# Performance work log

Measured on AMD Instinct MI355X. Metric: run time of the kernel, lower is better.

Reference implementation:

```python
import jax, jax.numpy as jnp
import numpy as np

B, N, D, H = 2, 512, 256, 256  # batch, seq_len, input_dim, hidden_dim
H2 = H // 2


def setup_inputs() -> dict:
    key = jax.random.key(0)
    ks = jax.random.split(key, 12)
    def lin(kw, kb, fan_in, fan_out):
        bound = 1.0 / np.sqrt(fan_in)
        W = jax.random.uniform(kw, (fan_in, fan_out), jnp.float32, -bound, bound)
        b = jax.random.uniform(kb, (fan_out,), jnp.float32, -bound, bound)
        return W, b
    W1, b1 = lin(ks[0], ks[1], 2 * D, H)
    W2, b2 = lin(ks[2], ks[3], H, H2)
    W3, b3 = lin(ks[4], ks[5], H2, 1)
    Wg, bg = lin(ks[6], ks[7], D, H)
    x = jax.random.normal(ks[8], (B, N, D), jnp.float32)
    base_adj = jax.random.uniform(ks[9], (B, N, N), jnp.float32)
    return {"x": x, "base_adj": base_adj, "W1": W1, "b1": b1,
            "W2": W2, "b2": b2, "W3": W3, "b3": b3, "Wg": Wg, "bg": bg}


def reference(x, base_adj, W1, b1, W2, b2, W3, b3, Wg, bg):
    # x: [B,N,D], base_adj: [B,N,N]
    Din = x.shape[-1]
    n = x.shape[1]
    # Linear on concat([x_i, x_j]) == x_i @ W1[:D] + x_j @ W1[D:]  (same math,
    # avoids materializing the [B,N,N,2D] pair tensor)
    left = jnp.einsum('bid,dh->bih', x, W1[:Din])    # [B,N,H]
    right = jnp.einsum('bjd,dh->bjh', x, W1[Din:])   # [B,N,H]
    h = jax.nn.relu(left[:, :, None, :] + right[:, None, :, :] + b1)  # [B,N,N,H]
    h = jax.nn.relu(jnp.einsum('bijh,hk->bijk', h, W2) + b2)          # [B,N,N,H/2]
    edge_weights = jax.nn.sigmoid(jnp.einsum('bijk,k->bij', h, W3[:, 0]) + b3[0])
    dynamic_adj = base_adj * edge_weights + jnp.eye(n, dtype=x.dtype)[None]
    dynamic_adj = jax.nn.softmax(dynamic_adj, axis=-1)
    agg = jnp.matmul(dynamic_adj, x)                 # [B,N,D]
    return jnp.einsum('bnd,dh->bnh', agg, Wg) + bg   # [B,N,H]
```

## Files before the change

### kernel.cpp

```cpp
#include <hip/hip_runtime.h>
#include <hip/hip_bf16.h>

#define NB 2
#define NN 512
#define ND 256
#define NH 256
#define NH2 128

#define JT 128
#define PADH 264

typedef __bf16 bf16x8 __attribute__((ext_vector_type(8)));
typedef float f32x4 __attribute__((ext_vector_type(4)));

__global__ __launch_bounds__(256) void prep_kernel(
    const float* __restrict__ x, const float* __restrict__ W1,
    const float* __restrict__ b1, const float* __restrict__ Wg,
    const float* __restrict__ bg, const float* __restrict__ W2,
    float* __restrict__ Lb, float* __restrict__ Rr, float* __restrict__ XW,
    __bf16* __restrict__ W2b) {
  const int blk = blockIdx.x;
  const int tid = threadIdx.x;
  if (blk >= 512) {
    const int idx = (blk - 512) * 256 + tid;
    const int k = idx >> 8;
    const int h = idx & 255;
    W2b[idx] = (__bf16)W2[h * NH2 + k];
    return;
  }
  __shared__ float xs[2][ND];
  const int r0 = blk * 2;
  xs[0][tid] = x[r0 * ND + tid];
  xs[1][tid] = x[(r0 + 1) * ND + tid];
  __syncthreads();

  float aL0 = 0.f, aL1 = 0.f, aR0 = 0.f, aR1 = 0.f, aG0 = 0.f, aG1 = 0.f;
  const int h = tid;
  for (int d = 0; d < ND; ++d) {
    const float wl = W1[d * NH + h];
    const float wr = W1[(ND + d) * NH + h];
    const float wg = Wg[d * NH + h];
    const float x0 = xs[0][d], x1 = xs[1][d];
    aL0 = fmaf(x0, wl, aL0); aL1 = fmaf(x1, wl, aL1);
    aR0 = fmaf(x0, wr, aR0); aR1 = fmaf(x1, wr, aR1);
    aG0 = fmaf(x0, wg, aG0); aG1 = fmaf(x1, wg, aG1);
  }
  const float bb1 = b1[h];
  const float bbg = bg[h];
  Lb[r0 * NH + h] = aL0 + bb1;       Lb[(r0 + 1) * NH + h] = aL1 + bb1;
  Rr[r0 * NH + h] = aR0;             Rr[(r0 + 1) * NH + h] = aR1;
  XW[r0 * NH + h] = aG0 + bbg;       XW[(r0 + 1) * NH + h] = aG1 + bbg;
}

__global__ __launch_bounds__(256, 2) void edge_kernel(
    const float* __restrict__ base_adj,
    const float* __restrict__ b2, const float* __restrict__ W3,
    const float* __restrict__ b3, const float* __restrict__ Lb,
    const float* __restrict__ Rr, const float* __restrict__ XW,
    const __bf16* __restrict__ W2b, float* __restrict__ out) {
  __shared__ __align__(16) __bf16 Hs[JT][PADH];
  __shared__ __align__(16) float Lbs[NH];
  __shared__ float b2s[NH2], W3s[NH2];
  __shared__ float ew[NN];
  __shared__ float red[2][JT];
  __shared__ float sred[8];

  const int bi = blockIdx.x;
  const int b = bi >> 9;
  const int i = bi & (NN - 1);
  const int tid = threadIdx.x;
  const int lane = tid & 63;
  const int w = tid >> 6;
  const int wy = w >> 1;
  const int wx = w & 1;
  const int lr = lane & 15;
  const int lg = lane >> 4;

  bf16x8 bfr[8][4];
  #pragma unroll
  for (int ks8 = 0; ks8 < 8; ++ks8)
    #pragma unroll
    for (int kb = 0; kb < 4; ++kb) {
      const int col = wx * 64 + kb * 16 + lr;
      bfr[ks8][kb] = *(const bf16x8*)(W2b + col * NH + ks8 * 32 + lg * 8);
    }

  Lbs[tid] = Lb[bi * NH + tid];
  if (tid < NH2) { b2s[tid] = b2[tid]; W3s[tid] = W3[tid]; }
  __syncthreads();

  const float* Rb = Rr + b * NN * NH;
  const float b3v = b3[0];

  for (int jt = 0; jt < NN; jt += JT) {
    #pragma unroll
    for (int it = 0; it < 16; ++it) {
      const int q = it * 256 + tid;
      const int jj = q >> 5;
      const int h8 = (q & 31) << 3;
      const f32x4 rv0 = *(const f32x4*)(Rb + (jt + jj) * NH + h8);
      const f32x4 rv1 = *(const f32x4*)(Rb + (jt + jj) * NH + h8 + 4);
      const f32x4 lv0 = *(const f32x4*)(Lbs + h8);
      const f32x4 lv1 = *(const f32x4*)(Lbs + h8 + 4);
      bf16x8 hv;
      #pragma unroll
      for (int e = 0; e < 4; ++e) {
        float t0 = rv0[e] + lv0[e];
        float t1 = rv1[e] + lv1[e];
        hv[e] = (__bf16)(t0 > 0.f ? t0 : 0.f);
        hv[e + 4] = (__bf16)(t1 > 0.f ? t1 : 0.f);
      }
      *(bf16x8*)(&Hs[jj][h8]) = hv;
    }
    __syncthreads();

    f32x4 acc[4][4];
    #pragma unroll
    for (int ja = 0; ja < 4; ++ja)
      #pragma unroll
      for (int kb = 0; kb < 4; ++kb) acc[ja][kb] = (f32x4){0.f, 0.f, 0.f, 0.f};

    const __bf16* Hp = &Hs[0][0];
    #pragma unroll
    for (int ks8 = 0; ks8 < 8; ++ks8) {
      bf16x8 af[4];
      #pragma unroll
      for (int ja = 0; ja < 4; ++ja) {
        const int row = wy * 64 + ja * 16 + lr;
        af[ja] = *(const bf16x8*)(Hp + row * PADH + ks8 * 32 + lg * 8);
      }
      #pragma unroll
      for (int ja = 0; ja < 4; ++ja)
        #pragma unroll
        for (int kb = 0; kb < 4; ++kb)
          acc[ja][kb] = __builtin_amdgcn_mfma_f32_16x16x32_bf16(af[ja], bfr[ks8][kb], acc[ja][kb], 0, 0, 0);
    }

    #pragma unroll
    for (int ja = 0; ja < 4; ++ja) {
      #pragma unroll
      for (int r = 0; r < 4; ++r) {
        float s = 0.f;
        #pragma unroll
        for (int kb = 0; kb < 4; ++kb) {
          const int k = wx * 64 + kb * 16 + lr;
          float t = acc[ja][kb][r] + b2s[k];
          t = t > 0.f ? t : 0.f;
          s = fmaf(t, W3s[k], s);
        }
        s += __shfl_xor(s, 1, 16);
        s += __shfl_xor(s, 2, 16);
        s += __shfl_xor(s, 4, 16);
        s += __shfl_xor(s, 8, 16);
        if (lr == 0) red[wx][wy * 64 + ja * 16 + lg * 4 + r] = s;
      }
    }
    __syncthreads();

    if (tid < JT) {
      const float v = red[0][tid] + red[1][tid] + b3v;
      const float sg = 1.f / (1.f + __expf(-v));
      const int j = jt + tid;
      ew[j] = base_adj[(b * NN + i) * NN + j] * sg + ((j == i) ? 1.f : 0.f);
    }
    __syncthreads();
  }

  float v0 = ew[tid], v1 = ew[tid + 256];
  float m = fmaxf(v0, v1);
  #pragma unroll
  for (int off = 1; off < 64; off <<= 1) m = fmaxf(m, __shfl_xor(m, off, 64));
  if (lane == 0) sred[w] = m;
  __syncthreads();
  m = fmaxf(fmaxf(sred[0], sred[1]), fmaxf(sred[2], sred[3]));
  const float e0 = __expf(v0 - m), e1 = __expf(v1 - m);
  float ssum = e0 + e1;
  #pragma unroll
  for (int off = 1; off < 64; off <<= 1) ssum += __shfl_xor(ssum, off, 64);
  if (lane == 0) sred[4 + w] = ssum;
  __syncthreads();
  const float inv = 1.f / (sred[4] + sred[5] + sred[6] + sred[7]);
  ew[tid] = e0 * inv;
  ew[tid + 256] = e1 * inv;
  __syncthreads();

  const float* XWb = XW + b * NN * NH;
  float o0 = 0.f, o1 = 0.f, o2 = 0.f, o3 = 0.f;
  for (int j = 0; j < NN; j += 4) {
    o0 = fmaf(ew[j + 0], XWb[(j + 0) * NH + tid], o0);
    o1 = fmaf(ew[j + 1], XWb[(j + 1) * NH + tid], o1);
    o2 = fmaf(ew[j + 2], XWb[(j + 2) * NH + tid], o2);
    o3 = fmaf(ew[j + 3], XWb[(j + 3) * NH + tid], o3);
  }
  out[bi * NH + tid] = (o0 + o1) + (o2 + o3);
}

extern "C" void kernel_launch(void* const* d_in, const int* in_sizes, int n_in,
                              void* d_out, int out_size, void* d_ws, size_t ws_size,
                              hipStream_t stream) {
  const float* x        = (const float*)d_in[0];
  const float* base_adj = (const float*)d_in[1];
  const float* W1       = (const float*)d_in[2];
  const float* b1       = (const float*)d_in[3];
  const float* W2       = (const float*)d_in[4];
  const float* b2       = (const float*)d_in[5];
  const float* W3       = (const float*)d_in[6];
  const float* b3       = (const float*)d_in[7];
  const float* Wg       = (const float*)d_in[8];
  const float* bg       = (const float*)d_in[9];

  float* Lb = (float*)d_ws;
  float* Rr = Lb + NB * NN * NH;
  float* XW = Rr + NB * NN * NH;
  __bf16* W2b = (__bf16*)(XW + NB * NN * NH);
  float* out = (float*)d_out;

  prep_kernel<<<512 + 128, 256, 0, stream>>>(x, W1, b1, Wg, bg, W2, Lb, Rr, XW, W2b);
  edge_kernel<<<NB * NN, 256, 0, stream>>>(base_adj, b2, W3, b3, Lb, Rr, XW, W2b, out);
}
```

Before: 202.5 us.

## Restructure edge kernel with bf16 intermediates, async LDS prefetch, smaller tiles

Stores the R projection and the XW aggregation operand as bf16, which halves their global traffic. The edge kernel now tiles j by 32 rows and double-buffers R tiles into LDS with global_load_lds prefetch, and it uses XOR-swizzled H rows to avoid bank conflicts. Each wave now owns a 32-column slice of the k dimension, which reduces register pressure so occupancy can rise to 4 blocks per CU. The prep kernel is vectorised over h with split-d partial sums, and base_adj is loaded up front. Rounding R and XW to bf16 adds some precision loss.

```diff
diff --git a/kernel.cpp b/kernel.cpp
--- a/kernel.cpp
+++ b/kernel.cpp
@@ -6,63 +6,105 @@
 #define ND 256
 #define NH 256
 #define NH2 128
-
-#define JT 128
-#define PADH 264
+#define JT 32
 
 typedef __bf16 bf16x8 __attribute__((ext_vector_type(8)));
+typedef __bf16 bf16x4 __attribute__((ext_vector_type(4)));
 typedef float f32x4 __attribute__((ext_vector_type(4)));
+
+__device__ __forceinline__ void gload_lds16(const void* g, void* l) {
+  __builtin_amdgcn_global_load_lds((const __attribute__((address_space(1))) unsigned int*)g,
+                                   (__attribute__((address_space(3))) unsigned int*)l, 16, 0, 0);
+}
+__device__ __forceinline__ float bflo(unsigned d) { return __uint_as_float(d << 16); }
+__device__ __forceinline__ float bfhi(unsigned d) { return __uint_as_float(d & 0xffff0000u); }
 
 __global__ __launch_bounds__(256) void prep_kernel(
     const float* __restrict__ x, const float* __restrict__ W1,
     const float* __restrict__ b1, const float* __restrict__ Wg,
     const float* __restrict__ bg, const float* __restrict__ W2,
-    float* __restrict__ Lb, float* __restrict__ Rr, float* __restrict__ XW,
-    __bf16* __restrict__ W2b) {
+    float* __restrict__ Lb, __bf16* __restrict__ Rb16,
+    __bf16* __restrict__ XWb16, __bf16* __restrict__ W2b) {
   const int blk = blockIdx.x;
   const int tid = threadIdx.x;
   if (blk >= 512) {
     const int idx = (blk - 512) * 256 + tid;
-    const int k = idx >> 8;
-    const int h = idx & 255;
-    W2b[idx] = (__bf16)W2[h * NH2 + k];
+    const int h = idx >> 7;
+    const int k = idx & 127;
+    W2b[k * NH + h] = (__bf16)W2[idx];
     return;
   }
   __shared__ float xs[2][ND];
+  __shared__ __align__(16) f32x4 part[4 * 384];
   const int r0 = blk * 2;
   xs[0][tid] = x[r0 * ND + tid];
   xs[1][tid] = x[(r0 + 1) * ND + tid];
   __syncthreads();
 
-  float aL0 = 0.f, aL1 = 0.f, aR0 = 0.f, aR1 = 0.f, aG0 = 0.f, aG1 = 0.f;
-  const int h = tid;
-  for (int d = 0; d < ND; ++d) {
-    const float wl = W1[d * NH + h];
-    const float wr = W1[(ND + d) * NH + h];
-    const float wg = Wg[d * NH + h];
+  const int dg = tid >> 6;
+  const int hq = tid & 63;
+  f32x4 acc[2][3];
+  #pragma unroll
+  for (int r = 0; r < 2; ++r)
+    #pragma unroll
+    for (int m = 0; m < 3; ++m) acc[r][m] = (f32x4){0.f, 0.f, 0.f, 0.f};
+
+  const int d0 = dg * 64;
+  for (int it = 0; it < 64; ++it) {
+    const int d = d0 + it;
+    const f32x4 wl = *(const f32x4*)(W1 + d * NH + hq * 4);
+    const f32x4 wr = *(const f32x4*)(W1 + (ND + d) * NH + hq * 4);
+    const f32x4 wg = *(const f32x4*)(Wg + d * NH + hq * 4);
     const float x0 = xs[0][d], x1 = xs[1][d];
-    aL0 = fmaf(x0, wl, aL0); aL1 = fmaf(x1, wl, aL1);
-    aR0 = fmaf(x0, wr, aR0); aR1 = fmaf(x1, wr, aR1);
-    aG0 = fmaf(x0, wg, aG0); aG1 = fmaf(x1, wg, aG1);
-  }
-  const float bb1 = b1[h];
-  const float bbg = bg[h];
-  Lb[r0 * NH + h] = aL0 + bb1;       Lb[(r0 + 1) * NH + h] = aL1 + bb1;
-  Rr[r0 * NH + h] = aR0;             Rr[(r0 + 1) * NH + h] = aR1;
-  XW[r0 * NH + h] = aG0 + bbg;       XW[(r0 + 1) * NH + h] = aG1 + bbg;
-}
-
-__global__ __launch_bounds__(256, 2) void edge_kernel(
+    acc[0][0] += x0 * wl;  acc[0][1] += x0 * wr;  acc[0][2] += x0 * wg;
+    acc[1][0] += x1 * wl;  acc[1][1] += x1 * wr;  acc[1][2] += x1 * wg;
+  }
+  #pragma unroll
+  for (int r = 0; r < 2; ++r)
+    #pragma unroll
+    for (int m = 0; m < 3; ++m)
+      part[dg * 384 + (r * 3 + m) * 64 + hq] = acc[r][m];
+  __syncthreads();
+
+  for (int s = tid; s < 384; s += 256) {
+    f32x4 sum = part[s] + part[384 + s] + part[768 + s] + part[1152 + s];
+    const int r = s / 192;
+    const int rem = s - r * 192;
+    const int m = rem >> 6;
+    const int h = (rem & 63) * 4;
+    const int row = r0 + r;
+    if (m == 0) {
+      const f32x4 bv = *(const f32x4*)(b1 + h);
+      *(f32x4*)(Lb + row * NH + h) = sum + bv;
+    } else if (m == 1) {
+      bf16x4 o;
+      #pragma unroll
+      for (int e = 0; e < 4; ++e) o[e] = (__bf16)sum[e];
+      *(bf16x4*)(Rb16 + row * NH + h) = o;
+    } else {
+      const f32x4 bv = *(const f32x4*)(bg + h);
+      const f32x4 v = sum + bv;
+      bf16x4 o;
+      #pragma unroll
+      for (int e = 0; e < 4; ++e) o[e] = (__bf16)v[e];
+      *(bf16x4*)(XWb16 + row * NH + h) = o;
+    }
+  }
+}
+
+__global__ __launch_bounds__(256, 4) void edge_kernel(
     const float* __restrict__ base_adj,
     const float* __restrict__ b2, const float* __restrict__ W3,
     const float* __restrict__ b3, const float* __restrict__ Lb,
-    const float* __restrict__ Rr, const float* __restrict__ XW,
+    const __bf16* __restrict__ Rb16, const __bf16* __restrict__ XWb16,
     const __bf16* __restrict__ W2b, float* __restrict__ out) {
-  __shared__ __align__(16) __bf16 Hs[JT][PADH];
+  __shared__ __align__(16) __bf16 Rs[JT * NH];
+  __shared__ __align__(16) __bf16 Hs[JT * NH];
   __shared__ __align__(16) float Lbs[NH];
+  __shared__ float adjs[NN];
+  __shared__ float ew[NN];
+  __shared__ float red[4][JT];
   __shared__ float b2s[NH2], W3s[NH2];
-  __shared__ float ew[NN];
-  __shared__ float red[2][JT];
   __shared__ float sred[8];
 
   const int bi = blockIdx.x;
@@ -71,100 +113,121 @@
   const int tid = threadIdx.x;
   const int lane = tid & 63;
   const int w = tid >> 6;
-  const int wy = w >> 1;
-  const int wx = w & 1;
   const int lr = lane & 15;
   const int lg = lane >> 4;
 
-  bf16x8 bfr[8][4];
+  const __bf16* Rbb = Rb16 + b * NN * NH;
+
+  {
+    const int laneoff = (lane >> 5) * NH + (lane & 31) * 8;
+    #pragma unroll
+    for (int q = 0; q < 4; ++q) {
+      const __bf16* src = Rbb + (w * 4 + q) * 2 * NH + laneoff;
+      gload_lds16(src, (char*)Rs + (w * 4 + q) * 1024);
+    }
+  }
+  bf16x8 bfr[8][2];
   #pragma unroll
   for (int ks8 = 0; ks8 < 8; ++ks8)
     #pragma unroll
-    for (int kb = 0; kb < 4; ++kb) {
-      const int col = wx * 64 + kb * 16 + lr;
-      bfr[ks8][kb] = *(const bf16x8*)(W2b + col * NH + ks8 * 32 + lg * 8);
-    }
-
+    for (int kb = 0; kb < 2; ++kb) {
+      const int k = w * 32 + kb * 16 + lr;
+      bfr[ks8][kb] = *(const bf16x8*)(W2b + k * NH + ks8 * 32 + lg * 8);
+    }
   Lbs[tid] = Lb[bi * NH + tid];
+  adjs[tid] = base_adj[(b * NN + i) * NN + tid];
+  adjs[tid + 256] = base_adj[(b * NN + i) * NN + tid + 256];
   if (tid < NH2) { b2s[tid] = b2[tid]; W3s[tid] = W3[tid]; }
-  __syncthreads();
-
-  const float* Rb = Rr + b * NN * NH;
   const float b3v = b3[0];
-
-  for (int jt = 0; jt < NN; jt += JT) {
-    #pragma unroll
-    for (int it = 0; it < 16; ++it) {
-      const int q = it * 256 + tid;
-      const int jj = q >> 5;
-      const int h8 = (q & 31) << 3;
-      const f32x4 rv0 = *(const f32x4*)(Rb + (jt + jj) * NH + h8);
-      const f32x4 rv1 = *(const f32x4*)(Rb + (jt + jj) * NH + h8 + 4);
-      const f32x4 lv0 = *(const f32x4*)(Lbs + h8);
-      const f32x4 lv1 = *(const f32x4*)(Lbs + h8 + 4);
-      bf16x8 hv;
+  asm volatile("s_waitcnt vmcnt(0)" ::: "memory");
+  __syncthreads();
+
+  const int cth = tid & 31;
+  float l8[8];
+  #pragma unroll
+  for (int e = 0; e < 8; ++e) l8[e] = Lbs[cth * 8 + e];
+  const int rowth = tid >> 5;
+  const unsigned rsAddr0 = tid * 16;
+  const unsigned hsAddr0 = rowth * 512 + ((cth ^ (rowth & 7)) << 4);
+
+  for (int jt = 0; jt < 16; ++jt) {
+    #pragma unroll
+    for (int it = 0; it < 4; ++it) {
+      const uint4 rv = *(const uint4*)((const char*)Rs + rsAddr0 + it * 4096);
+      bf16x8 hb;
       #pragma unroll
       for (int e = 0; e < 4; ++e) {
-        float t0 = rv0[e] + lv0[e];
-        float t1 = rv1[e] + lv1[e];
-        hv[e] = (__bf16)(t0 > 0.f ? t0 : 0.f);
-        hv[e + 4] = (__bf16)(t1 > 0.f ? t1 : 0.f);
-      }
-      *(bf16x8*)(&Hs[jj][h8]) = hv;
+        const unsigned d = ((const unsigned*)&rv)[e];
+        float t0 = bflo(d) + l8[2 * e];
+        float t1 = bfhi(d) + l8[2 * e + 1];
+        t0 = t0 > 0.f ? t0 : 0.f;
+        t1 = t1 > 0.f ? t1 : 0.f;
+        hb[2 * e] = (__bf16)t0;
+        hb[2 * e + 1] = (__bf16)t1;
+      }
+      *(bf16x8*)((char*)Hs + hsAddr0 + it * 4096) = hb;
     }
     __syncthreads();
 
-    f32x4 acc[4][4];
-    #pragma unroll
-    for (int ja = 0; ja < 4; ++ja)
-      #pragma unroll
-      for (int kb = 0; kb < 4; ++kb) acc[ja][kb] = (f32x4){0.f, 0.f, 0.f, 0.f};
-
-    const __bf16* Hp = &Hs[0][0];
+    if (jt < 15) {
+      const int laneoff = (lane >> 5) * NH + (lane & 31) * 8;
+      const __bf16* base = Rbb + (jt + 1) * (JT * NH);
+      #pragma unroll
+      for (int q = 0; q < 4; ++q) {
+        const __bf16* src = base + (w * 4 + q) * 2 * NH + laneoff;
+        gload_lds16(src, (char*)Rs + (w * 4 + q) * 1024);
+      }
+    }
+
+    f32x4 acc[2][2];
+    #pragma unroll
+    for (int ja = 0; ja < 2; ++ja)
+      #pragma unroll
+      for (int kb = 0; kb < 2; ++kb) acc[ja][kb] = (f32x4){0.f, 0.f, 0.f, 0.f};
     #pragma unroll
     for (int ks8 = 0; ks8 < 8; ++ks8) {
-      bf16x8 af[4];
-      #pragma unroll
-      for (int ja = 0; ja < 4; ++ja) {
-        const int row = wy * 64 + ja * 16 + lr;
-        af[ja] = *(const bf16x8*)(Hp + row * PADH + ks8 * 32 + lg * 8);
-      }
-      #pragma unroll
-      for (int ja = 0; ja < 4; ++ja)
+      bf16x8 af[2];
+      #pragma unroll
+      for (int ja = 0; ja < 2; ++ja) {
+        const int row = ja * 16 + lr;
+        const int c = (ks8 * 4 + lg) ^ (lr & 7);
+        af[ja] = *(const bf16x8*)((const char*)Hs + row * 512 + (c << 4));
+      }
+      #pragma unroll
+      for (int ja = 0; ja < 2; ++ja)
         #pragma unroll
-        for (int kb = 0; kb < 4; ++kb)
+        for (int kb = 0; kb < 2; ++kb)
           acc[ja][kb] = __builtin_amdgcn_mfma_f32_16x16x32_bf16(af[ja], bfr[ks8][kb], acc[ja][kb], 0, 0, 0);
     }
 
     #pragma unroll
-    for (int ja = 0; ja < 4; ++ja) {
+    for (int ja = 0; ja < 2; ++ja) {
       #pragma unroll
       for (int r = 0; r < 4; ++r) {
-        float s = 0.f;
-        #pragma unroll
-        for (int kb = 0; kb < 4; ++kb) {
-          const int k = wx * 64 + kb * 16 + lr;
-          float t = acc[ja][kb][r] + b2s[k];
-          t = t > 0.f ? t : 0.f;
-          s = fmaf(t, W3s[k], s);
-        }
+        const int k0 = w * 32 + lr;
+        float t0 = acc[ja][0][r] + b2s[k0];
+        float t1 = acc[ja][1][r] + b2s[k0 + 16];
+        t0 = t0 > 0.f ? t0 : 0.f;
+        t1 = t1 > 0.f ? t1 : 0.f;
+        float s = fmaf(t0, W3s[k0], t1 * W3s[k0 + 16]);
         s += __shfl_xor(s, 1, 16);
         s += __shfl_xor(s, 2, 16);
         s += __shfl_xor(s, 4, 16);
         s += __shfl_xor(s, 8, 16);
-        if (lr == 0) red[wx][wy * 64 + ja * 16 + lg * 4 + r] = s;
-      }
-    }
+        if (lr == 0) red[w][ja * 16 + lg * 4 + r] = s;
+      }
+    }
+    asm volatile("s_waitcnt vmcnt(0)" ::: "memory");
     __syncthreads();
 
     if (tid < JT) {
-      const float v = red[0][tid] + red[1][tid] + b3v;
+      const float v = red[0][tid] + red[1][tid] + red[2][tid] + red[3][tid] + b3v;
       const float sg = 1.f / (1.f + __expf(-v));
-      const int j = jt + tid;
-      ew[j] = base_adj[(b * NN + i) * NN + j] * sg + ((j == i) ? 1.f : 0.f);
-    }
-    __syncthreads();
-  }
+      const int j = jt * JT + tid;
+      ew[j] = adjs[j] * sg + ((j == i) ? 1.f : 0.f);
+    }
+  }
+  __syncthreads();
 
   float v0 = ew[tid], v1 = ew[tid + 256];
   float m = fmaxf(v0, v1);
@@ -184,15 +247,23 @@
   ew[tid + 256] = e1 * inv;
   __syncthreads();
 
-  const float* XWb = XW + b * NN * NH;
-  float o0 = 0.f, o1 = 0.f, o2 = 0.f, o3 = 0.f;
-  for (int j = 0; j < NN; j += 4) {
-    o0 = fmaf(ew[j + 0], XWb[(j + 0) * NH + tid], o0);
-    o1 = fmaf(ew[j + 1], XWb[(j + 1) * NH + tid], o1);
-    o2 = fmaf(ew[j + 2], XWb[(j + 2) * NH + tid], o2);
-    o3 = fmaf(ew[j + 3], XWb[(j + 3) * NH + tid], o3);
-  }
-  out[bi * NH + tid] = (o0 + o1) + (o2 + o3);
+  const int jg = tid >> 7;
+  const int h2 = tid & 127;
+  const unsigned* Xp = (const unsigned*)(XWb16 + b * NN * NH) + jg * 256 * 128 + h2;
+  float a0 = 0.f, a1 = 0.f, c0 = 0.f, c1 = 0.f;
+  for (int jj = 0; jj < 256; jj += 2) {
+    const int j0 = jg * 256 + jj;
+    const unsigned d0 = Xp[jj * 128];
+    const unsigned d1 = Xp[jj * 128 + 128];
+    const float p0 = ew[j0], p1 = ew[j0 + 1];
+    a0 = fmaf(p0, bflo(d0), a0);  a1 = fmaf(p0, bfhi(d0), a1);
+    c0 = fmaf(p1, bflo(d1), c0);  c1 = fmaf(p1, bfhi(d1), c1);
+  }
+  float* pv = adjs;
+  pv[jg * 256 + h2 * 2] = a0 + c0;
+  pv[jg * 256 + h2 * 2 + 1] = a1 + c1;
+  __syncthreads();
+  out[bi * NH + tid] = pv[tid] + pv[256 + tid];
 }
 
 extern "C" void kernel_launch(void* const* d_in, const int* in_sizes, int n_in,
@@ -209,12 +280,12 @@
   const float* Wg       = (const float*)d_in[8];
   const float* bg       = (const float*)d_in[9];
 
-  float* Lb = (float*)d_ws;
-  float* Rr = Lb + NB * NN * NH;
-  float* XW = Rr + NB * NN * NH;
-  __bf16* W2b = (__bf16*)(XW + NB * NN * NH);
-  float* out = (float*)d_out;
-
-  prep_kernel<<<512 + 128, 256, 0, stream>>>(x, W1, b1, Wg, bg, W2, Lb, Rr, XW, W2b);
-  edge_kernel<<<NB * NN, 256, 0, stream>>>(base_adj, b2, W3, b3, Lb, Rr, XW, W2b, out);
-}
+  float*  Lb    = (float*)d_ws;
+  __bf16* Rb16  = (__bf16*)(Lb + NB * NN * NH);
+  __bf16* XWb16 = Rb16 + NB * NN * NH;
+  __bf16* W2b   = XWb16 + NB * NN * NH;
+  float* outp = (float*)d_out;
+
+  prep_kernel<<<640, 256, 0, stream>>>(x, W1, b1, Wg, bg, W2, Lb, Rb16, XWb16, W2b);
+  edge_kernel<<<NB * NN, 256, 0, stream>>>(base_adj, b2, W3, b3, Lb, Rb16, XWb16, W2b, outp);
+}
```

New measurement: 163.3 us. 19.4% less time.
